# Kernel tuning notes

Hardware: AMD Instinct MI355X
Metric: run time of the kernel (lower is better)

Reference implementation:

```python
import jax, jax.numpy as jnp
import numpy as np

INPUT_DIM = (480, 640)


def _lstm_dir(x, Wih, Whh, b, reverse):
    # x: [B, T, I]; Wih: [4H, I]; Whh: [4H, H]; b: [4H] (= b_ih + b_hh)
    # PyTorch gate order: i, f, g, o
    B = x.shape[0]
    H = Whh.shape[1]
    gx = jnp.einsum('bti,gi->btg', x, Wih) + b  # input projection for all steps

    def step(carry, g):
        h, c = carry
        g = g + h @ Whh.T
        i, f, gg, o = jnp.split(g, 4, axis=-1)
        c = jax.nn.sigmoid(f) * c + jax.nn.sigmoid(i) * jnp.tanh(gg)
        h = jax.nn.sigmoid(o) * jnp.tanh(c)
        return (h, c), h

    init = (jnp.zeros((B, H), x.dtype), jnp.zeros((B, H), x.dtype))
    _, hs = jax.lax.scan(step, init, gx.transpose(1, 0, 2), reverse=reverse)
    return hs.transpose(1, 0, 2)  # [B, T, H], aligned to input positions


def _bilstm(x, Wih, Whh, b):
    fwd = _lstm_dir(x, Wih[0], Whh[0], b[0], False)
    bwd = _lstm_dir(x, Wih[1], Whh[1], b[1], True)
    return jnp.concatenate([fwd, bwd], axis=-1)


def _scan_rows(x, sc, Wih, Whh, b):
    # x: [N, H, W, C]; sc added at first/last column of every row (scene-context fusion)
    N, Hh, Ww, C = x.shape
    x = x.at[:, :, 0, :].add(sc[:, None, :]).at[:, :, -1, :].add(sc[:, None, :])
    y = _bilstm(x.reshape(N * Hh, Ww, C), Wih, Whh, b)  # all rows batched together
    return y.reshape(N, Hh, Ww, -1)


def _scan_cols(x, sc, Wih, Whh, b):
    N, Hh, Ww, C = x.shape
    x = x.at[:, 0, :, :].add(sc[:, None, :]).at[:, -1, :, :].add(sc[:, None, :])
    xt = x.transpose(0, 2, 1, 3).reshape(N * Ww, Hh, C)  # all cols batched together
    y = _bilstm(xt, Wih, Whh, b)
    return y.reshape(N, Ww, Hh, -1).transpose(0, 2, 1, 3)


def _upsample_ac(x, out_hw):
    # bilinear resize with align_corners=True; x: [N, C, h, w]
    N, C, h, w = x.shape
    oh, ow = out_hw

    def coords(n_in, n_out):
        s = jnp.arange(n_out, dtype=x.dtype) * ((n_in - 1) / (n_out - 1))
        i0 = jnp.clip(jnp.floor(s).astype(jnp.int32), 0, n_in - 2)
        return i0, s - i0.astype(x.dtype)

    y0, ty = coords(h, oh)
    x0, tx = coords(w, ow)
    g = x[:, :, y0, :] * (1 - ty)[None, None, :, None] + x[:, :, y0 + 1, :] * ty[None, None, :, None]
    g = g[:, :, :, x0] * (1 - tx) + g[:, :, :, x0 + 1] * tx
    return g


def setup_inputs() -> dict:
    key = jax.random.key(0)
    ks = jax.random.split(key, 16)
    N, Hl, Wl = 8, 60, 80
    HS = 128
    G = 4 * HS

    def w(k, shape, scale=0.05):
        return jax.random.normal(k, shape, jnp.float32) * scale

    def lstm_params(k, I):
        k1, k2, k3 = jax.random.split(k, 3)
        Wih = w(k1, (2, G, I))
        Whh = w(k2, (2, G, HS))
        # forget-gate bias filled with 1.0 in both b_ih and b_hh -> 2.0 combined
        b = w(k3, (2, G)).at[:, HS:2 * HS].set(2.0)
        return Wih, Whh, b

    h1 = lstm_params(ks[0], 512)
    v1 = lstm_params(ks[1], 256)
    h2 = lstm_params(ks[2], 256)
    v2 = lstm_params(ks[3], 256)
    return {
        'local_feats': jax.random.normal(ks[4], (N, 512, Hl, Wl), jnp.float32),
        'scene_ctx': jax.random.normal(ks[5], (N, 128), jnp.float32),
        'fc1_w': w(ks[6], (512, 128)), 'fc1_b': w(ks[7], (512,)),
        'fcr_w': w(ks[8], (256, 128)), 'fcr_b': w(ks[9], (256,)),
        'h1_wih': h1[0], 'h1_whh': h1[1], 'h1_b': h1[2],
        'v1_wih': v1[0], 'v1_whh': v1[1], 'v1_b': v1[2],
        'h2_wih': h2[0], 'h2_whh': h2[1], 'h2_b': h2[2],
        'v2_wih': v2[0], 'v2_whh': v2[1], 'v2_b': v2[2],
        'conv_w': w(ks[10], (1, 256)), 'conv_b': w(ks[11], (1,)),
    }


def reference(local_feats, scene_ctx, fc1_w, fc1_b, fcr_w, fcr_b,
              h1_wih, h1_whh, h1_b, v1_wih, v1_whh, v1_b,
              h2_wih, h2_whh, h2_b, v2_wih, v2_whh, v2_b,
              conv_w, conv_b):
    lf = local_feats.transpose(0, 2, 3, 1)  # [N, H, W, 512]
    sc1 = scene_ctx @ fc1_w.T + fc1_b       # [N, 512] (scene_context_fc_1)
    scr = scene_ctx @ fcr_w.T + fcr_b       # [N, 256] (scene_context_fc_rest)
    x = _scan_rows(lf, sc1, h1_wih, h1_whh, h1_b)   # H-BLSTM 1
    x = _scan_cols(x, scr, v1_wih, v1_whh, v1_b)    # V-BLSTM 1
    x = _scan_rows(x, scr, h2_wih, h2_whh, h2_b)    # H-BLSTM 2
    x = _scan_cols(x, scr, v2_wih, v2_whh, v2_b)    # V-BLSTM 2
    logits = jnp.einsum('nhwc,oc->nohw', x, conv_w) + conv_b[None, :, None, None]
    score = jax.nn.sigmoid(logits)
    return _upsample_ac(score, INPUT_DIM)
```

## Files before the change

kernel.cpp:

```cpp
#include <hip/hip_runtime.h>
#include <hip/hip_bf16.h>
#include <math.h>


#define NIMG 8
#define PTOT 38400
#define PADH 136

typedef _Float16 half8 __attribute__((ext_vector_type(8)));
typedef _Float16 half4 __attribute__((ext_vector_type(4)));
typedef float float4v __attribute__((ext_vector_type(4)));
typedef __attribute__((address_space(1))) const void gvoid_t;
typedef __attribute__((address_space(3))) void svoid_t;

__device__ __forceinline__ void gload16(void* s, const void* g) {
  __builtin_amdgcn_global_load_lds((gvoid_t*)g, (svoid_t*)s, 16, 0, 0);
}
__device__ __forceinline__ void lds_barrier() {
  __asm__ volatile("s_waitcnt lgkmcnt(0)\n\ts_barrier" ::: "memory");
}

__device__ __forceinline__ float rcp_(float x) { return __builtin_amdgcn_rcpf(x); }
__device__ __forceinline__ float fsig(float x) { return rcp_(1.f + __expf(-x)); }
__device__ __forceinline__ float ftanh_(float x) {
  float e = __expf(-2.f * x);
  return 2.f * rcp_(1.f + e) - 1.f;
}

__global__ void k_fc(const float* __restrict__ ctx, const float* __restrict__ w1,
                     const float* __restrict__ b1, const float* __restrict__ wr,
                     const float* __restrict__ br, float* __restrict__ sc1,
                     float* __restrict__ scr) {
  int n = blockIdx.x;
  __shared__ float c[128];
  int t = threadIdx.x;
  if (t < 128) c[t] = ctx[n * 128 + t];
  __syncthreads();
  if (t < 512) {
    float a = b1[t];
    const float* wp = w1 + t * 128;
    for (int k = 0; k < 128; k++) a += wp[k] * c[k];
    sc1[n * 512 + t] = a;
  } else {
    int j = t - 512;
    float a = br[j];
    const float* wp = wr + j * 128;
    for (int k = 0; k < 128; k++) a += wp[k] * c[k];
    scr[n * 256 + j] = a;
  }
}

__global__ void k_hfrag(const float* __restrict__ whh, _Float16* __restrict__ out) {
  int idx = blockIdx.x * 512 + threadIdx.x;
  int j = idx & 7, lane = (idx >> 3) & 63, kt = (idx >> 9) & 3;
  int G = (idx >> 11) & 3, w = (idx >> 13) & 7, dir = idx >> 16;
  int n = G * 128 + w * 16 + (lane & 15);
  int k = kt * 32 + (lane >> 4) * 8 + j;
  out[idx] = (_Float16)whh[(dir * 512 + n) * 128 + k];
}

__global__ void k_wpermpack(const float* __restrict__ in, _Float16* __restrict__ out,
                            int K) {
  int idx = blockIdx.x * 512 + threadIdx.x;
  int np = idx / K, k = idx - np * K;
  int orig = (np & 512) + (np & 3) * 128 + ((np & 511) >> 2);
  out[(size_t)np * K + k] = (_Float16)in[(size_t)orig * K + k];
}

__global__ void k_prep1(const float* __restrict__ lf, const float* __restrict__ sc1,
                        _Float16* __restrict__ x) {
  __shared__ float tile[32][33];
  int n = blockIdx.z;
  int p0 = blockIdx.x * 32;
  int i0 = blockIdx.y * 32;
  const float* src = lf + (size_t)n * 512 * 4800;
  for (int r = threadIdx.y; r < 32; r += 8)
    tile[r][threadIdx.x] = src[(size_t)(i0 + r) * 4800 + p0 + threadIdx.x];
  __syncthreads();
  for (int r = threadIdx.y; r < 32; r += 8) {
    int p = p0 + r;
    int w = p % 80;
    int ch = i0 + threadIdx.x;
    float v = tile[threadIdx.x][r];
    if (w == 0 || w == 79) v += sc1[n * 512 + ch];
    x[((size_t)n * 4800 + p) * 512 + ch] = (_Float16)v;
  }
}

__global__ void k_swap(const _Float16* __restrict__ y, const float* __restrict__ sc,
                       _Float16* __restrict__ x, int A, int B) {
  int b = blockIdx.x, a = blockIdx.y, n = blockIdx.z, c = threadIdx.x;
  float v = (float)y[(((size_t)n * A + a) * B + b) * 256 + c];
  if (a == 0 || a == A - 1) v += sc[n * 256 + c];
  x[(((size_t)n * B + b) * A + a) * 256 + c] = (_Float16)v;
}

__global__ __launch_bounds__(256) void k_gemm_h(const _Float16* __restrict__ A,
                                                const _Float16* __restrict__ W,
                                                const float* __restrict__ bias,
                                                _Float16* __restrict__ C, int K) {
  __shared__ _Float16 As[128 * 32];
  __shared__ _Float16 Bs[128 * 32];
  int bm = blockIdx.x * 128, bn = blockIdx.y * 128;
  int tid = threadIdx.x;
  int w = tid >> 6, lane = tid & 63;
  int ln = lane & 15, quad = lane >> 4;
  int Wm = (w >> 1) * 64, Wn = (w & 1) * 64;
  int srow = w * 16 + (lane >> 2);
  int scol = (lane & 3) * 8;
  const _Float16* Ap0 = A + (size_t)(bm + srow) * K + scol;
  const _Float16* Ap1 = A + (size_t)(bm + 64 + srow) * K + scol;
  const _Float16* Bp0 = W + (size_t)(bn + srow) * K + scol;
  const _Float16* Bp1 = W + (size_t)(bn + 64 + srow) * K + scol;
  _Float16* sA0 = As + (w * 16) * 32;
  _Float16* sA1 = As + (64 + w * 16) * 32;
  _Float16* sB0 = Bs + (w * 16) * 32;
  _Float16* sB1 = Bs + (64 + w * 16) * 32;

  float4v acc[4][4];
#pragma unroll
  for (int i = 0; i < 4; i++)
#pragma unroll
    for (int j = 0; j < 4; j++) acc[i][j] = (float4v){0.f, 0.f, 0.f, 0.f};

  for (int k0 = 0; k0 < K; k0 += 32) {
    gload16(sA0, Ap0 + k0);
    gload16(sA1, Ap1 + k0);
    gload16(sB0, Bp0 + k0);
    gload16(sB1, Bp1 + k0);
    __syncthreads();
    const _Float16* ar = As + (Wm + ln) * 32 + quad * 8;
    const _Float16* br = Bs + (Wn + ln) * 32 + quad * 8;
    half8 af[4], bf_[4];
#pragma unroll
    for (int mt = 0; mt < 4; mt++) af[mt] = *(const half8*)(ar + mt * 512);
#pragma unroll
    for (int nt = 0; nt < 4; nt++) bf_[nt] = *(const half8*)(br + nt * 512);
#pragma unroll
    for (int mt = 0; mt < 4; mt++)
#pragma unroll
      for (int nt = 0; nt < 4; nt++)
        acc[mt][nt] = __builtin_amdgcn_mfma_f32_16x16x32_f16(af[mt], bf_[nt],
                                                             acc[mt][nt], 0, 0, 0);
    __syncthreads();
  }
#pragma unroll
  for (int nt = 0; nt < 4; nt++) {
    int col = bn + Wn + nt * 16 + ln;
    int orig = (col & 512) + (col & 3) * 128 + ((col & 511) >> 2);
    float bv = bias[orig];
#pragma unroll
    for (int mt = 0; mt < 4; mt++) {
      size_t rbase = (size_t)(bm + Wm + mt * 16 + quad * 4) * 1024 + col;
#pragma unroll
      for (int r = 0; r < 4; r++)
        C[rbase + (size_t)r * 1024] = (_Float16)(acc[mt][nt][r] + bv);
    }
  }
}

__device__ __forceinline__ void lstm_step(const half4* g, const half8 bfrag[4][4],
                                          const _Float16* hread, _Float16* hwrite,
                                          _Float16* yp, size_t yrstride,
                                          float* c, int ln, int quad, int u,
                                          bool act) {
  half8 af[4];
  const _Float16* hp = hread + ln * PADH + quad * 8;
#pragma unroll
  for (int kt = 0; kt < 4; kt++) af[kt] = *(const half8*)(hp + kt * 32);
  float4v acc[4];
#pragma unroll
  for (int G = 0; G < 4; G++) {
    float4v a = {(float)g[0][G], (float)g[1][G], (float)g[2][G], (float)g[3][G]};
#pragma unroll
    for (int kt = 0; kt < 4; kt++)
      a = __builtin_amdgcn_mfma_f32_16x16x32_f16(af[kt], bfrag[G][kt], a, 0, 0, 0);
    acc[G] = a;
  }
#pragma unroll
  for (int r = 0; r < 4; r++) {
    float iv = fsig(acc[0][r]);
    float fv = fsig(acc[1][r]);
    float gv = ftanh_(acc[2][r]);
    float ov = fsig(acc[3][r]);
    c[r] = fv * c[r] + iv * gv;
    float hv = ov * ftanh_(c[r]);
    if (act) {
      hwrite[(quad * 4 + r) * PADH + u] = (_Float16)hv;
      yp[r * yrstride] = (_Float16)hv;
    }
  }
  lds_barrier();
}

__global__ __launch_bounds__(512, 2) void k_lstm2(const _Float16* __restrict__ gx,
                                                  const _Float16* __restrict__ bfr,
                                                  _Float16* __restrict__ y, int T) {
  int dir = blockIdx.y;
  int s0 = blockIdx.x * 8;
  int tid = threadIdx.x;
  int w = tid >> 6;
  int lane = tid & 63;
  int ln = lane & 15, quad = lane >> 4;
  int u = w * 16 + ln;
  bool act = quad < 2;

  __shared__ __align__(16) _Float16 hbuf[2][16 * PADH];

  half8 bfrag[4][4];
  const _Float16* bp = bfr + ((size_t)dir * 8 + w) * 8192;
#pragma unroll
  for (int G = 0; G < 4; G++)
#pragma unroll
    for (int kt = 0; kt < 4; kt++)
      bfrag[G][kt] = *(const half8*)(bp + ((G * 4 + kt) * 64 + lane) * 8);

  for (int i = tid; i < 2 * 16 * PADH; i += 512) ((_Float16*)hbuf)[i] = (_Float16)0.f;

  float c[4] = {0.f, 0.f, 0.f, 0.f};
  int srow = s0 + quad * 4;
  const _Float16* gbase = gx + ((size_t)(act ? srow : s0) * T) * 1024 + dir * 512 + u * 4;
  size_t sstride = (size_t)T * 1024;
  size_t ystride = (size_t)T * 256;

  half4 gA[4] = {}, gB[4] = {};
  {
    int t0 = dir ? (T - 1) : 0;
    if (act)
#pragma unroll
      for (int r = 0; r < 4; r++)
        gA[r] = *(const half4*)(gbase + r * sstride + (size_t)t0 * 1024);
  }
  lds_barrier();

  for (int st = 0; st < T; st += 2) {
    int t = dir ? (T - 1 - st) : st;
    int t1 = dir ? (T - 2 - st) : st + 1;
    if (act)
#pragma unroll
      for (int r = 0; r < 4; r++)
        gB[r] = *(const half4*)(gbase + r * sstride + (size_t)t1 * 1024);
    lstm_step(gA, bfrag, hbuf[0], hbuf[1],
              y + ((size_t)(act ? srow : s0) * T + t) * 256 + dir * 128 + u,
              ystride, c, ln, quad, u, act);
    if (st + 2 < T && act) {
      int t2 = dir ? (T - 3 - st) : st + 2;
#pragma unroll
      for (int r = 0; r < 4; r++)
        gA[r] = *(const half4*)(gbase + r * sstride + (size_t)t2 * 1024);
    }
    lstm_step(gB, bfrag, hbuf[1], hbuf[0],
              y + ((size_t)(act ? srow : s0) * T + t1) * 256 + dir * 128 + u,
              ystride, c, ln, quad, u, act);
  }
}

__global__ void k_head(const _Float16* __restrict__ y, const float* __restrict__ cw,
                       const float* __restrict__ cb, float* __restrict__ score) {
  int wv = threadIdx.x >> 6, ln = threadIdx.x & 63;
  int o = blockIdx.x * 4 + wv;
  const _Float16* yp = y + (size_t)o * 256;
  float a = 0.f;
  for (int c = ln; c < 256; c += 64) a += (float)yp[c] * cw[c];
  for (int off = 32; off; off >>= 1) a += __shfl_down(a, off);
  if (ln == 0) {
    int h = o % 60;
    int nw = o / 60;
    int w = nw % 80;
    int n = nw / 80;
    score[(n * 60 + h) * 80 + w] = fsig(a + cb[0]);
  }
}

__global__ void k_up(const float* __restrict__ score, float* __restrict__ out) {
  int idx = blockIdx.x * 256 + threadIdx.x;
  if (idx >= NIMG * 480 * 640) return;
  int ox = idx % 640;
  int t = idx / 640;
  int oy = t % 480;
  int n = t / 480;
  float sy = oy * (59.f / 479.f);
  float sx = ox * (79.f / 639.f);
  int y0 = min((int)sy, 58);
  int x0 = min((int)sx, 78);
  float ty = sy - (float)y0;
  float tx = sx - (float)x0;
  const float* sp = score + n * 4800;
  float v00 = sp[y0 * 80 + x0], v01 = sp[y0 * 80 + x0 + 1];
  float v10 = sp[(y0 + 1) * 80 + x0], v11 = sp[(y0 + 1) * 80 + x0 + 1];
  float v0 = v00 + (v01 - v00) * tx;
  float v1 = v10 + (v11 - v10) * tx;
  out[idx] = v0 + (v1 - v0) * ty;
}

extern "C" void kernel_launch(void* const* d_in, const int* in_sizes, int n_in,
                              void* d_out, int out_size, void* d_ws, size_t ws_size,
                              hipStream_t stream) {
  const float* lf    = (const float*)d_in[0];
  const float* ctx   = (const float*)d_in[1];
  const float* fc1w  = (const float*)d_in[2];
  const float* fc1b  = (const float*)d_in[3];
  const float* fcrw  = (const float*)d_in[4];
  const float* fcrb  = (const float*)d_in[5];
  const float* wih[4] = {(const float*)d_in[6], (const float*)d_in[9],
                         (const float*)d_in[12], (const float*)d_in[15]};
  const float* whh[4] = {(const float*)d_in[7], (const float*)d_in[10],
                         (const float*)d_in[13], (const float*)d_in[16]};
  const float* bb[4]  = {(const float*)d_in[8], (const float*)d_in[11],
                         (const float*)d_in[14], (const float*)d_in[17]};
  const float* convw = (const float*)d_in[18];
  const float* convb = (const float*)d_in[19];
  float* out = (float*)d_out;

  float* ws    = (float*)d_ws;
  float* sc1   = ws;
  float* scr   = ws + 4096;
  float* score = ws + 6144;
  _Float16* hb = (_Float16*)(ws + 44544);
  _Float16* hfr  = hb;
  _Float16* wpk  = hb + 524288;
  _Float16* xbuf = hb + 1835008;
  _Float16* gxh  = hb + 21495808;
  _Float16* ybuf = hb + 60817408;
  _Float16* wpkL[4] = {wpk, wpk + 524288, wpk + 786432, wpk + 1048576};

  k_fc<<<NIMG, 768, 0, stream>>>(ctx, fc1w, fc1b, fcrw, fcrb, sc1, scr);
  for (int l = 0; l < 4; l++)
    k_hfrag<<<256, 512, 0, stream>>>(whh[l], hfr + (size_t)l * 131072);
  k_wpermpack<<<1024, 512, 0, stream>>>(wih[0], wpkL[0], 512);
  for (int l = 1; l < 4; l++)
    k_wpermpack<<<512, 512, 0, stream>>>(wih[l], wpkL[l], 256);
  k_prep1<<<dim3(150, 16, NIMG), dim3(32, 8), 0, stream>>>(lf, sc1, xbuf);

  k_gemm_h<<<dim3(300, 8), 256, 0, stream>>>(xbuf, wpkL[0], bb[0], gxh, 512);
  k_lstm2<<<dim3(60, 2), 512, 0, stream>>>(gxh, hfr + 0 * 131072, ybuf, 80);

  k_swap<<<dim3(80, 60, NIMG), 256, 0, stream>>>(ybuf, scr, xbuf, 60, 80);
  k_gemm_h<<<dim3(300, 8), 256, 0, stream>>>(xbuf, wpkL[1], bb[1], gxh, 256);
  k_lstm2<<<dim3(80, 2), 512, 0, stream>>>(gxh, hfr + 1 * 131072, ybuf, 60);

  k_swap<<<dim3(60, 80, NIMG), 256, 0, stream>>>(ybuf, scr, xbuf, 80, 60);
  k_gemm_h<<<dim3(300, 8), 256, 0, stream>>>(xbuf, wpkL[2], bb[2], gxh, 256);
  k_lstm2<<<dim3(60, 2), 512, 0, stream>>>(gxh, hfr + 2 * 131072, ybuf, 80);

  k_swap<<<dim3(80, 60, NIMG), 256, 0, stream>>>(ybuf, scr, xbuf, 60, 80);
  k_gemm_h<<<dim3(300, 8), 256, 0, stream>>>(xbuf, wpkL[3], bb[3], gxh, 256);
  k_lstm2<<<dim3(80, 2), 512, 0, stream>>>(gxh, hfr + 3 * 131072, ybuf, 60);

  k_head<<<PTOT / 4, 256, 0, stream>>>(ybuf, convw, convb, score);
  k_up<<<(NIMG * 480 * 640 + 255) / 256, 256, 0, stream>>>(score, out);
}
```

Before: 800.9 us.

## Fuse transpose and context add into LSTM; process 32 sequences per block

```diff
diff --git a/kernel.cpp b/kernel.cpp
--- a/kernel.cpp
+++ b/kernel.cpp
@@ -85,14 +85,6 @@
     if (w == 0 || w == 79) v += sc1[n * 512 + ch];
     x[((size_t)n * 4800 + p) * 512 + ch] = (_Float16)v;
   }
-}
-
-__global__ void k_swap(const _Float16* __restrict__ y, const float* __restrict__ sc,
-                       _Float16* __restrict__ x, int A, int B) {
-  int b = blockIdx.x, a = blockIdx.y, n = blockIdx.z, c = threadIdx.x;
-  float v = (float)y[(((size_t)n * A + a) * B + b) * 256 + c];
-  if (a == 0 || a == A - 1) v += sc[n * 256 + c];
-  x[(((size_t)n * B + b) * A + a) * 256 + c] = (_Float16)v;
 }
 
 __global__ __launch_bounds__(256) void k_gemm_h(const _Float16* __restrict__ A,
@@ -159,53 +151,19 @@
   }
 }
 
-__device__ __forceinline__ void lstm_step(const half4* g, const half8 bfrag[4][4],
-                                          const _Float16* hread, _Float16* hwrite,
-                                          _Float16* yp, size_t yrstride,
-                                          float* c, int ln, int quad, int u,
-                                          bool act) {
-  half8 af[4];
-  const _Float16* hp = hread + ln * PADH + quad * 8;
-#pragma unroll
-  for (int kt = 0; kt < 4; kt++) af[kt] = *(const half8*)(hp + kt * 32);
-  float4v acc[4];
-#pragma unroll
-  for (int G = 0; G < 4; G++) {
-    float4v a = {(float)g[0][G], (float)g[1][G], (float)g[2][G], (float)g[3][G]};
-#pragma unroll
-    for (int kt = 0; kt < 4; kt++)
-      a = __builtin_amdgcn_mfma_f32_16x16x32_f16(af[kt], bfrag[G][kt], a, 0, 0, 0);
-    acc[G] = a;
-  }
-#pragma unroll
-  for (int r = 0; r < 4; r++) {
-    float iv = fsig(acc[0][r]);
-    float fv = fsig(acc[1][r]);
-    float gv = ftanh_(acc[2][r]);
-    float ov = fsig(acc[3][r]);
-    c[r] = fv * c[r] + iv * gv;
-    float hv = ov * ftanh_(c[r]);
-    if (act) {
-      hwrite[(quad * 4 + r) * PADH + u] = (_Float16)hv;
-      yp[r * yrstride] = (_Float16)hv;
-    }
-  }
-  lds_barrier();
-}
-
-__global__ __launch_bounds__(512, 2) void k_lstm2(const _Float16* __restrict__ gx,
+__global__ __launch_bounds__(512, 2) void k_lstm3(const _Float16* __restrict__ gx,
                                                   const _Float16* __restrict__ bfr,
-                                                  _Float16* __restrict__ y, int T) {
+                                                  _Float16* __restrict__ outp,
+                                                  const float* __restrict__ scr,
+                                                  int T, int S, int swap_mode) {
   int dir = blockIdx.y;
-  int s0 = blockIdx.x * 8;
+  int s0 = blockIdx.x * 32;
   int tid = threadIdx.x;
-  int w = tid >> 6;
-  int lane = tid & 63;
+  int w = tid >> 6, lane = tid & 63;
   int ln = lane & 15, quad = lane >> 4;
   int u = w * 16 + ln;
-  bool act = quad < 2;
-
-  __shared__ __align__(16) _Float16 hbuf[2][16 * PADH];
+
+  __shared__ __align__(16) _Float16 hbuf[2][2][16 * PADH];
 
   half8 bfrag[4][4];
   const _Float16* bp = bfr + ((size_t)dir * 8 + w) * 8192;
@@ -215,43 +173,98 @@
     for (int kt = 0; kt < 4; kt++)
       bfrag[G][kt] = *(const half8*)(bp + ((G * 4 + kt) * 64 + lane) * 8);
 
-  for (int i = tid; i < 2 * 16 * PADH; i += 512) ((_Float16*)hbuf)[i] = (_Float16)0.f;
-
-  float c[4] = {0.f, 0.f, 0.f, 0.f};
-  int srow = s0 + quad * 4;
-  const _Float16* gbase = gx + ((size_t)(act ? srow : s0) * T) * 1024 + dir * 512 + u * 4;
+  for (int i = tid; i < 2 * 2 * 16 * PADH; i += 512)
+    ((_Float16*)hbuf)[i] = (_Float16)0.f;
+
+  float cst[2][4] = {};
+  const _Float16* gbase[2];
+  _Float16* ob[2][4];
+  float scrv[2][4];
   size_t sstride = (size_t)T * 1024;
-  size_t ystride = (size_t)T * 256;
-
-  half4 gA[4] = {}, gB[4] = {};
+  size_t ostride = (size_t)(swap_mode ? S : 1) * 256;
+#pragma unroll
+  for (int g = 0; g < 2; g++) {
+    int srow = s0 + g * 16 + quad * 4;
+    gbase[g] = gx + (size_t)srow * sstride + dir * 512 + u * 4;
+#pragma unroll
+    for (int r = 0; r < 4; r++) {
+      int seq = srow + r;
+      if (swap_mode) {
+        int n = seq / S, rem = seq - n * S;
+        ob[g][r] = outp + ((size_t)n * T * S + rem) * 256 + dir * 128 + u;
+        scrv[g][r] = (rem == 0 || rem == S - 1) ? scr[n * 256 + dir * 128 + u] : 0.f;
+      } else {
+        ob[g][r] = outp + (size_t)seq * T * 256 + dir * 128 + u;
+        scrv[g][r] = 0.f;
+      }
+    }
+  }
+
+  half4 gA[2][4], gB[2][4];
   {
     int t0 = dir ? (T - 1) : 0;
-    if (act)
-#pragma unroll
-      for (int r = 0; r < 4; r++)
-        gA[r] = *(const half4*)(gbase + r * sstride + (size_t)t0 * 1024);
+    int t1 = dir ? (T - 2) : 1;
+#pragma unroll
+    for (int g = 0; g < 2; g++)
+#pragma unroll
+      for (int r = 0; r < 4; r++) {
+        gA[g][r] = *(const half4*)(gbase[g] + r * sstride + (size_t)t0 * 1024);
+        gB[g][r] = *(const half4*)(gbase[g] + r * sstride + (size_t)t1 * 1024);
+      }
   }
   lds_barrier();
 
+  const _Float16* hrd = &hbuf[0][0][ln * PADH + quad * 8];
+  const int grpoff = 2 * 16 * PADH;
+
+  auto step = [&](half4 (&gg)[2][4], int st, half4 (&gp)[2][4]) {
+    int t = dir ? (T - 1 - st) : st;
+    int pb = st & 1;
+    half8 af[2][4];
+#pragma unroll
+    for (int g = 0; g < 2; g++)
+#pragma unroll
+      for (int kt = 0; kt < 4; kt++)
+        af[g][kt] = *(const half8*)(hrd + g * grpoff + pb * 16 * PADH + kt * 32);
+    float4v acc[2][4];
+#pragma unroll
+    for (int G = 0; G < 4; G++)
+#pragma unroll
+      for (int g = 0; g < 2; g++) {
+        float4v a = {(float)gg[g][0][G], (float)gg[g][1][G],
+                     (float)gg[g][2][G], (float)gg[g][3][G]};
+#pragma unroll
+        for (int kt = 0; kt < 4; kt++)
+          a = __builtin_amdgcn_mfma_f32_16x16x32_f16(af[g][kt], bfrag[G][kt], a, 0, 0, 0);
+        acc[g][G] = a;
+      }
+    if (st + 2 < T) {
+      int tn = dir ? (T - 3 - st) : (st + 2);
+#pragma unroll
+      for (int g = 0; g < 2; g++)
+#pragma unroll
+        for (int r = 0; r < 4; r++)
+          gp[g][r] = *(const half4*)(gbase[g] + r * sstride + (size_t)tn * 1024);
+    }
+#pragma unroll
+    for (int g = 0; g < 2; g++)
+#pragma unroll
+      for (int r = 0; r < 4; r++) {
+        float iv = fsig(acc[g][0][r]);
+        float fv = fsig(acc[g][1][r]);
+        float gv = ftanh_(acc[g][2][r]);
+        float ov = fsig(acc[g][3][r]);
+        cst[g][r] = fv * cst[g][r] + iv * gv;
+        float hv = ov * ftanh_(cst[g][r]);
+        hbuf[g][1 - pb][(quad * 4 + r) * PADH + u] = (_Float16)hv;
+        ob[g][r][(size_t)t * ostride] = (_Float16)(hv + scrv[g][r]);
+      }
+    lds_barrier();
+  };
+
   for (int st = 0; st < T; st += 2) {
-    int t = dir ? (T - 1 - st) : st;
-    int t1 = dir ? (T - 2 - st) : st + 1;
-    if (act)
-#pragma unroll
-      for (int r = 0; r < 4; r++)
-        gB[r] = *(const half4*)(gbase + r * sstride + (size_t)t1 * 1024);
-    lstm_step(gA, bfrag, hbuf[0], hbuf[1],
-              y + ((size_t)(act ? srow : s0) * T + t) * 256 + dir * 128 + u,
-              ystride, c, ln, quad, u, act);
-    if (st + 2 < T && act) {
-      int t2 = dir ? (T - 3 - st) : st + 2;
-#pragma unroll
-      for (int r = 0; r < 4; r++)
-        gA[r] = *(const half4*)(gbase + r * sstride + (size_t)t2 * 1024);
-    }
-    lstm_step(gB, bfrag, hbuf[1], hbuf[0],
-              y + ((size_t)(act ? srow : s0) * T + t1) * 256 + dir * 128 + u,
-              ystride, c, ln, quad, u, act);
+    step(gA, st, gA);
+    step(gB, st + 1, gB);
   }
 }
 
@@ -333,19 +346,16 @@
   k_prep1<<<dim3(150, 16, NIMG), dim3(32, 8), 0, stream>>>(lf, sc1, xbuf);
 
   k_gemm_h<<<dim3(300, 8), 256, 0, stream>>>(xbuf, wpkL[0], bb[0], gxh, 512);
-  k_lstm2<<<dim3(60, 2), 512, 0, stream>>>(gxh, hfr + 0 * 131072, ybuf, 80);
-
-  k_swap<<<dim3(80, 60, NIMG), 256, 0, stream>>>(ybuf, scr, xbuf, 60, 80);
+  k_lstm3<<<dim3(15, 2), 512, 0, stream>>>(gxh, hfr + 0 * 131072, xbuf, scr, 80, 60, 1);
+
   k_gemm_h<<<dim3(300, 8), 256, 0, stream>>>(xbuf, wpkL[1], bb[1], gxh, 256);
-  k_lstm2<<<dim3(80, 2), 512, 0, stream>>>(gxh, hfr + 1 * 131072, ybuf, 60);
-
-  k_swap<<<dim3(60, 80, NIMG), 256, 0, stream>>>(ybuf, scr, xbuf, 80, 60);
+  k_lstm3<<<dim3(20, 2), 512, 0, stream>>>(gxh, hfr + 1 * 131072, xbuf, scr, 60, 80, 1);
+
   k_gemm_h<<<dim3(300, 8), 256, 0, stream>>>(xbuf, wpkL[2], bb[2], gxh, 256);
-  k_lstm2<<<dim3(60, 2), 512, 0, stream>>>(gxh, hfr + 2 * 131072, ybuf, 80);
-
-  k_swap<<<dim3(80, 60, NIMG), 256, 0, stream>>>(ybuf, scr, xbuf, 60, 80);
+  k_lstm3<<<dim3(15, 2), 512, 0, stream>>>(gxh, hfr + 2 * 131072, xbuf, scr, 80, 60, 1);
+
   k_gemm_h<<<dim3(300, 8), 256, 0, stream>>>(xbuf, wpkL[3], bb[3], gxh, 256);
-  k_lstm2<<<dim3(80, 2), 512, 0, stream>>>(gxh, hfr + 3 * 131072, ybuf, 60);
+  k_lstm3<<<dim3(20, 2), 512, 0, stream>>>(gxh, hfr + 3 * 131072, ybuf, scr, 60, 80, 0);
 
   k_head<<<PTOT / 4, 256, 0, stream>>>(ybuf, convw, convb, score);
   k_up<<<(NIMG * 480 * 640 + 255) / 256, 256, 0, stream>>>(score, out);
```

Result: slower. 955.9 us (+19.4%).

## Fuse transpose and scene-context add into LSTM output; use all 16 MFMA rows

Applied to the files above, without the earlier changes.

```diff
diff --git a/kernel.cpp b/kernel.cpp
--- a/kernel.cpp
+++ b/kernel.cpp
@@ -85,14 +85,6 @@
     if (w == 0 || w == 79) v += sc1[n * 512 + ch];
     x[((size_t)n * 4800 + p) * 512 + ch] = (_Float16)v;
   }
-}
-
-__global__ void k_swap(const _Float16* __restrict__ y, const float* __restrict__ sc,
-                       _Float16* __restrict__ x, int A, int B) {
-  int b = blockIdx.x, a = blockIdx.y, n = blockIdx.z, c = threadIdx.x;
-  float v = (float)y[(((size_t)n * A + a) * B + b) * 256 + c];
-  if (a == 0 || a == A - 1) v += sc[n * 256 + c];
-  x[(((size_t)n * B + b) * A + a) * 256 + c] = (_Float16)v;
 }
 
 __global__ __launch_bounds__(256) void k_gemm_h(const _Float16* __restrict__ A,
@@ -159,51 +151,17 @@
   }
 }
 
-__device__ __forceinline__ void lstm_step(const half4* g, const half8 bfrag[4][4],
-                                          const _Float16* hread, _Float16* hwrite,
-                                          _Float16* yp, size_t yrstride,
-                                          float* c, int ln, int quad, int u,
-                                          bool act) {
-  half8 af[4];
-  const _Float16* hp = hread + ln * PADH + quad * 8;
-#pragma unroll
-  for (int kt = 0; kt < 4; kt++) af[kt] = *(const half8*)(hp + kt * 32);
-  float4v acc[4];
-#pragma unroll
-  for (int G = 0; G < 4; G++) {
-    float4v a = {(float)g[0][G], (float)g[1][G], (float)g[2][G], (float)g[3][G]};
-#pragma unroll
-    for (int kt = 0; kt < 4; kt++)
-      a = __builtin_amdgcn_mfma_f32_16x16x32_f16(af[kt], bfrag[G][kt], a, 0, 0, 0);
-    acc[G] = a;
-  }
-#pragma unroll
-  for (int r = 0; r < 4; r++) {
-    float iv = fsig(acc[0][r]);
-    float fv = fsig(acc[1][r]);
-    float gv = ftanh_(acc[2][r]);
-    float ov = fsig(acc[3][r]);
-    c[r] = fv * c[r] + iv * gv;
-    float hv = ov * ftanh_(c[r]);
-    if (act) {
-      hwrite[(quad * 4 + r) * PADH + u] = (_Float16)hv;
-      yp[r * yrstride] = (_Float16)hv;
-    }
-  }
-  lds_barrier();
-}
-
-__global__ __launch_bounds__(512, 2) void k_lstm2(const _Float16* __restrict__ gx,
+__global__ __launch_bounds__(512, 2) void k_lstm4(const _Float16* __restrict__ gx,
                                                   const _Float16* __restrict__ bfr,
-                                                  _Float16* __restrict__ y, int T) {
+                                                  _Float16* __restrict__ outp,
+                                                  const float* __restrict__ scr,
+                                                  int T, int S, int swap_mode) {
   int dir = blockIdx.y;
-  int s0 = blockIdx.x * 8;
+  int s0 = blockIdx.x * 16;
   int tid = threadIdx.x;
-  int w = tid >> 6;
-  int lane = tid & 63;
+  int w = tid >> 6, lane = tid & 63;
   int ln = lane & 15, quad = lane >> 4;
   int u = w * 16 + ln;
-  bool act = quad < 2;
 
   __shared__ __align__(16) _Float16 hbuf[2][16 * PADH];
 
@@ -215,43 +173,85 @@
     for (int kt = 0; kt < 4; kt++)
       bfrag[G][kt] = *(const half8*)(bp + ((G * 4 + kt) * 64 + lane) * 8);
 
-  for (int i = tid; i < 2 * 16 * PADH; i += 512) ((_Float16*)hbuf)[i] = (_Float16)0.f;
-
-  float c[4] = {0.f, 0.f, 0.f, 0.f};
+  for (int i = tid; i < 2 * 16 * PADH; i += 512)
+    ((_Float16*)hbuf)[i] = (_Float16)0.f;
+
+  float cst[4] = {0.f, 0.f, 0.f, 0.f};
   int srow = s0 + quad * 4;
-  const _Float16* gbase = gx + ((size_t)(act ? srow : s0) * T) * 1024 + dir * 512 + u * 4;
+  const _Float16* gbase = gx + (size_t)srow * T * 1024 + dir * 512 + u * 4;
   size_t sstride = (size_t)T * 1024;
-  size_t ystride = (size_t)T * 256;
-
-  half4 gA[4] = {}, gB[4] = {};
+  size_t ostride = (size_t)(swap_mode ? S : 1) * 256;
+  _Float16* ob[4];
+  float scrv[4];
+#pragma unroll
+  for (int r = 0; r < 4; r++) {
+    int seq = srow + r;
+    if (swap_mode) {
+      int n = seq / S, rem = seq - n * S;
+      ob[r] = outp + ((size_t)n * T * S + rem) * 256 + dir * 128 + u;
+      scrv[r] = (rem == 0 || rem == S - 1) ? scr[n * 256 + dir * 128 + u] : 0.f;
+    } else {
+      ob[r] = outp + (size_t)seq * T * 256 + dir * 128 + u;
+      scrv[r] = 0.f;
+    }
+  }
+
+  half4 gA[4], gB[4];
   {
     int t0 = dir ? (T - 1) : 0;
-    if (act)
+#pragma unroll
+    for (int r = 0; r < 4; r++)
+      gA[r] = *(const half4*)(gbase + r * sstride + (size_t)t0 * 1024);
+  }
+  lds_barrier();
+
+  const _Float16* hrd = &hbuf[0][ln * PADH + quad * 8];
+
+  auto step = [&](half4 (&gg)[4], int st, half4 (&gp)[4], bool pf) {
+    int t = dir ? (T - 1 - st) : st;
+    int pb = st & 1;
+    half8 af[4];
+#pragma unroll
+    for (int kt = 0; kt < 4; kt++)
+      af[kt] = *(const half8*)(hrd + pb * 16 * PADH + kt * 32);
+    float4v acc[4];
+#pragma unroll
+    for (int G = 0; G < 4; G++) {
+      float4v a = {(float)gg[0][G], (float)gg[1][G], (float)gg[2][G], (float)gg[3][G]};
+#pragma unroll
+      for (int kt = 0; kt < 4; kt++)
+        a = __builtin_amdgcn_mfma_f32_16x16x32_f16(af[kt], bfrag[G][kt], a, 0, 0, 0);
+      acc[G] = a;
+    }
+    if (pf) {
+      int tn = dir ? (T - 3 - st) : (st + 2);
 #pragma unroll
       for (int r = 0; r < 4; r++)
-        gA[r] = *(const half4*)(gbase + r * sstride + (size_t)t0 * 1024);
-  }
-  lds_barrier();
-
+        gp[r] = *(const half4*)(gbase + r * sstride + (size_t)tn * 1024);
+    }
+#pragma unroll
+    for (int r = 0; r < 4; r++) {
+      float iv = fsig(acc[0][r]);
+      float fv = fsig(acc[1][r]);
+      float gv = ftanh_(acc[2][r]);
+      float ov = fsig(acc[3][r]);
+      cst[r] = fv * cst[r] + iv * gv;
+      float hv = ov * ftanh_(cst[r]);
+      hbuf[1 - pb][(quad * 4 + r) * PADH + u] = (_Float16)hv;
+      ob[r][(size_t)t * ostride] = (_Float16)(hv + scrv[r]);
+    }
+    lds_barrier();
+  };
+
+  {
+    int t1 = dir ? (T - 2) : 1;
+#pragma unroll
+    for (int r = 0; r < 4; r++)
+      gB[r] = *(const half4*)(gbase + r * sstride + (size_t)t1 * 1024);
+  }
   for (int st = 0; st < T; st += 2) {
-    int t = dir ? (T - 1 - st) : st;
-    int t1 = dir ? (T - 2 - st) : st + 1;
-    if (act)
-#pragma unroll
-      for (int r = 0; r < 4; r++)
-        gB[r] = *(const half4*)(gbase + r * sstride + (size_t)t1 * 1024);
-    lstm_step(gA, bfrag, hbuf[0], hbuf[1],
-              y + ((size_t)(act ? srow : s0) * T + t) * 256 + dir * 128 + u,
-              ystride, c, ln, quad, u, act);
-    if (st + 2 < T && act) {
-      int t2 = dir ? (T - 3 - st) : st + 2;
-#pragma unroll
-      for (int r = 0; r < 4; r++)
-        gA[r] = *(const half4*)(gbase + r * sstride + (size_t)t2 * 1024);
-    }
-    lstm_step(gB, bfrag, hbuf[1], hbuf[0],
-              y + ((size_t)(act ? srow : s0) * T + t1) * 256 + dir * 128 + u,
-              ystride, c, ln, quad, u, act);
+    step(gA, st, gA, st + 2 < T);
+    step(gB, st + 1, gB, st + 3 < T);
   }
 }
 
@@ -333,19 +333,16 @@
   k_prep1<<<dim3(150, 16, NIMG), dim3(32, 8), 0, stream>>>(lf, sc1, xbuf);
 
   k_gemm_h<<<dim3(300, 8), 256, 0, stream>>>(xbuf, wpkL[0], bb[0], gxh, 512);
-  k_lstm2<<<dim3(60, 2), 512, 0, stream>>>(gxh, hfr + 0 * 131072, ybuf, 80);
-
-  k_swap<<<dim3(80, 60, NIMG), 256, 0, stream>>>(ybuf, scr, xbuf, 60, 80);
+  k_lstm4<<<dim3(30, 2), 512, 0, stream>>>(gxh, hfr + 0 * 131072, xbuf, scr, 80, 60, 1);
+
   k_gemm_h<<<dim3(300, 8), 256, 0, stream>>>(xbuf, wpkL[1], bb[1], gxh, 256);
-  k_lstm2<<<dim3(80, 2), 512, 0, stream>>>(gxh, hfr + 1 * 131072, ybuf, 60);
-
-  k_swap<<<dim3(60, 80, NIMG), 256, 0, stream>>>(ybuf, scr, xbuf, 80, 60);
+  k_lstm4<<<dim3(40, 2), 512, 0, stream>>>(gxh, hfr + 1 * 131072, xbuf, scr, 60, 80, 1);
+
   k_gemm_h<<<dim3(300, 8), 256, 0, stream>>>(xbuf, wpkL[2], bb[2], gxh, 256);
-  k_lstm2<<<dim3(60, 2), 512, 0, stream>>>(gxh, hfr + 2 * 131072, ybuf, 80);
-
-  k_swap<<<dim3(80, 60, NIMG), 256, 0, stream>>>(ybuf, scr, xbuf, 60, 80);
+  k_lstm4<<<dim3(30, 2), 512, 0, stream>>>(gxh, hfr + 2 * 131072, xbuf, scr, 80, 60, 1);
+
   k_gemm_h<<<dim3(300, 8), 256, 0, stream>>>(xbuf, wpkL[3], bb[3], gxh, 256);
-  k_lstm2<<<dim3(80, 2), 512, 0, stream>>>(gxh, hfr + 3 * 131072, ybuf, 60);
+  k_lstm4<<<dim3(40, 2), 512, 0, stream>>>(gxh, hfr + 3 * 131072, ybuf, scr, 60, 80, 0);
 
   k_head<<<PTOT / 4, 256, 0, stream>>>(ybuf, convw, convb, score);
   k_up<<<(NIMG * 480 * 640 + 255) / 256, 256, 0, stream>>>(score, out);
```

Measured after the change: 711.5 us. 11.2% less time.
